# Performance work log

Measured on AMD Instinct MI355X. Metric: run time of the kernel, lower is better.

The kernel has to match this reference:

```python
import jax, jax.numpy as jnp
import numpy as np

MUL = 8              # multiplicity of 0e and 1o irreps (feature dim = MUL + 3*MUL = 32)
N_NODES = 25000
N_EDGES = 200000
EDGE_ATTR_DIM = 16
RADIAL_HIDDEN = 64
N_PATHS = 5          # CG paths: 0e*0e->0e, 0e*1o->1o, 1o*0e->1o, 1o*1o->0e, 1o*1o->1o


def _split(x):
    # x: [*, MUL + 3*MUL] -> scalars [*, MUL], vectors [*, MUL, 3]
    return x[:, :MUL], x[:, MUL:].reshape(x.shape[0], MUL, 3)


def _radial(edge_attr, W1, W2):
    # two-layer radial net (e3nn FullyConnectedNet style, silu, fan-in normalized)
    h = jax.nn.silu(edge_attr @ W1 / jnp.sqrt(float(EDGE_ATTR_DIM)))
    w = h @ W2 / jnp.sqrt(float(RADIAL_HIDDEN))
    return w.reshape(-1, N_PATHS, MUL, MUL)  # [E, 5, MUL, MUL]


def _edge_tp(xs, xv, s0, s1, w):
    # per-edge FullyConnectedTensorProduct(irreps_in, irreps_sh, irreps_out)
    # xs:[E,MUL] xv:[E,MUL,3] s0:[E] s1:[E,3] w:[E,5,MUL,MUL]
    dot = jnp.einsum('emc,ec->em', xv, s1) / jnp.sqrt(3.0)          # 1o x 1o -> 0e
    out_s = (jnp.einsum('emn,em->en', w[:, 0], xs) * s0[:, None]
             + jnp.einsum('emn,em->en', w[:, 3], dot)) / jnp.sqrt(2.0 * MUL)
    cross = jnp.cross(xv, s1[:, None, :]) / jnp.sqrt(2.0)            # 1o x 1o -> 1o
    out_v = (jnp.einsum('emn,em->en', w[:, 1], xs)[:, :, None] * s1[:, None, :]
             + jnp.einsum('emn,emc->enc', w[:, 2], xv) * s0[:, None, None]
             + jnp.einsum('emn,emc->enc', w[:, 4], cross)) / jnp.sqrt(3.0 * MUL)
    return out_s, out_v


def setup_inputs() -> dict:
    key = jax.random.key(0)
    ks = jax.random.split(key, 12)
    node_attr = jax.random.normal(ks[0], (N_NODES, 4 * MUL), jnp.float32)
    edge_index = jax.random.randint(ks[1], (2, N_EDGES), 0, N_NODES, dtype=jnp.int32)
    edge_attr = jax.random.normal(ks[2], (N_EDGES, EDGE_ATTR_DIM), jnp.float32)
    edge_sh = jax.random.normal(ks[3], (N_EDGES, 4), jnp.float32)
    WSZ = N_PATHS * MUL * MUL
    return {
        'node_attr': node_attr,
        'edge_index': edge_index,
        'edge_attr': edge_attr,
        'edge_sh': edge_sh,
        'Wq0': jax.random.normal(ks[4], (MUL, MUL), jnp.float32),
        'Wq1': jax.random.normal(ks[5], (MUL, MUL), jnp.float32),
        'kW1': jax.random.normal(ks[6], (EDGE_ATTR_DIM, RADIAL_HIDDEN), jnp.float32),
        'kW2': jax.random.normal(ks[7], (RADIAL_HIDDEN, WSZ), jnp.float32),
        'vW1': jax.random.normal(ks[8], (EDGE_ATTR_DIM, RADIAL_HIDDEN), jnp.float32),
        'vW2': jax.random.normal(ks[9], (RADIAL_HIDDEN, WSZ), jnp.float32),
        'Wd0': jax.random.normal(ks[10], (MUL, MUL), jnp.float32),
        'Wd1': jax.random.normal(ks[11], (MUL, MUL), jnp.float32),
    }


def reference(node_attr, edge_index, edge_attr, edge_sh,
              Wq0, Wq1, kW1, kW2, vW1, vW2, Wd0, Wd1):
    src, dst = edge_index[0], edge_index[1]
    inv_sqrt_mul = 1.0 / jnp.sqrt(float(MUL))

    # q = o3.Linear(irreps_in -> irreps_query): mixes multiplicities within each irrep
    ns, nv = _split(node_attr)
    qs = ns @ Wq0 * inv_sqrt_mul                                   # [N, MUL]
    qv = jnp.einsum('nmc,mk->nkc', nv, Wq1) * inv_sqrt_mul          # [N, MUL, 3]

    # per-edge keys/values: gather src features, tensor product with edge_sh
    xs, xv = ns[src], nv[src]
    s0, s1 = edge_sh[:, 0], edge_sh[:, 1:4]
    wk = _radial(edge_attr, kW1, kW2)
    wv = _radial(edge_attr, vW1, vW2)
    ks_, kv_ = _edge_tp(xs, xv, s0, s1, wk)
    vs_, vv_ = _edge_tp(xs, xv, s0, s1, wv)

    # dot = FullyConnectedTensorProduct(query, key, '0e') per edge
    logits = (jnp.einsum('mn,em,en->e', Wd0, qs[dst], ks_)
              + jnp.einsum('mn,emc,enc->e', Wd1, qv[dst], kv_) / jnp.sqrt(3.0)
              ) / jnp.sqrt(2.0 * MUL)
    exp = jnp.exp(logits)[:, None]                                 # [E, 1]

    # scatter-mean normalization
    z_sum = jax.ops.segment_sum(exp, dst, num_segments=N_NODES)
    cnt = jax.ops.segment_sum(jnp.ones_like(exp), dst, num_segments=N_NODES)
    z = z_sum / jnp.maximum(cnt, 1.0)
    alpha = exp / z[dst]
    attn = jnp.sqrt(jax.nn.relu(alpha))

    # weighted scatter-sum aggregation
    v_edge = jnp.concatenate([vs_, vv_.reshape(-1, 3 * MUL)], axis=1)  # [E, 32]
    out = jax.ops.segment_sum(attn * v_edge, dst, num_segments=N_NODES)
    return out
```

## Files before the change

### kernel.cpp

```cpp
#include <hip/hip_runtime.h>
#include <math.h>

#define NE 200000
#define NN 25000

static constexpr float INV_SQRT3  = 0.5773502691896258f;
static constexpr float INV_SQRT2  = 0.7071067811865476f;
static constexpr float INV_SQRT8  = 0.3535533905932738f;
static constexpr float INV_SQRT24 = 0.2041241452319315f;

typedef __attribute__((ext_vector_type(8))) short bf16x8;
typedef __attribute__((ext_vector_type(4))) float f32x4;

union U16x8 { uint4 u; bf16x8 v; };

__device__ __forceinline__ unsigned f2bf1(float f) {
  unsigned u = __float_as_uint(f);
  return (u + 0x7FFFu + ((u >> 16) & 1u)) >> 16;
}
__device__ __forceinline__ unsigned packbf(float a, float b) {
  return f2bf1(a) | (f2bf1(b) << 16);
}
__device__ __forceinline__ float bflo(unsigned u) { return __uint_as_float(u << 16); }
__device__ __forceinline__ float bfhi(unsigned u) { return __uint_as_float(u & 0xFFFF0000u); }

__global__ __launch_bounds__(256) void prep_kernel(
    const float* __restrict__ kW1, const float* __restrict__ kW2,
    const float* __restrict__ vW1, const float* __restrict__ vW2,
    const float* __restrict__ node_attr,
    const float* __restrict__ Wq0, const float* __restrict__ Wq1,
    const float* __restrict__ Wd0, const float* __restrict__ Wd1,
    const int*   __restrict__ edge_index,
    unsigned short* __restrict__ afrag,
    unsigned short* __restrict__ afrag1,
    float* __restrict__ qd, float* __restrict__ qvd,
    int* __restrict__ hist)
{
  int t = blockIdx.x * blockDim.x + threadIdx.x;
  if (t < 4096) {
    int j    = t & 7;
    int lane = (t >> 3) & 63;
    int rt   = (t >> 9) & 3;
    int b    = (t >> 11) & 1;
    int quad = lane >> 4;
    int k    = quad * 8 + j;
    int jeff = k & 15;
    int r    = rt * 16 + (lane & 15);
    const float* W = b ? vW1 : kW1;
    afrag1[t] = (unsigned short)f2bf1(W[jeff * 64 + r]);
  }
  if (t < 40960) {
    int j    = t & 7;
    int lane = (t >> 3) & 63;
    int kk   = (t >> 9) & 1;
    int ot   = (t >> 10) & 1;
    int ci   = t >> 11;
    int b    = ci / 10;
    int rem  = ci - b * 10;
    int p    = rem >> 1;
    int hf   = rem & 1;
    int r    = kk * 32 + ((lane >> 4) << 3) + j;
    int o    = p * 64 + hf * 32 + ot * 16 + (lane & 15);
    const float* W = b ? vW2 : kW2;
    afrag[t] = (unsigned short)f2bf1(W[r * 320 + o]);
  }
#pragma unroll
  for (int i = 0; i < 5; ++i) {
    int e = t * 5 + i;
    if (e < NE) atomicAdd(&hist[edge_index[NE + e]], 1);
  }
  if (t < NN) {
    int n = t;
    float ns[8], nv[24];
#pragma unroll
    for (int i = 0; i < 8; ++i)  ns[i] = node_attr[n * 32 + i];
#pragma unroll
    for (int i = 0; i < 24; ++i) nv[i] = node_attr[n * 32 + 8 + i];
    float qs[8];
#pragma unroll
    for (int m = 0; m < 8; ++m) {
      float a = 0.f;
#pragma unroll
      for (int i = 0; i < 8; ++i) a = fmaf(ns[i], Wq0[i * 8 + m], a);
      qs[m] = a * INV_SQRT8;
    }
#pragma unroll
    for (int k = 0; k < 8; ++k) {
      float a = 0.f;
#pragma unroll
      for (int m = 0; m < 8; ++m) a = fmaf(qs[m], Wd0[m * 8 + k], a);
      qd[n * 8 + k] = a;
    }
    float qv[24];
#pragma unroll
    for (int k = 0; k < 8; ++k) {
#pragma unroll
      for (int c = 0; c < 3; ++c) {
        float a = 0.f;
#pragma unroll
        for (int m = 0; m < 8; ++m) a = fmaf(nv[m * 3 + c], Wq1[m * 8 + k], a);
        qv[k * 3 + c] = a * INV_SQRT8;
      }
    }
#pragma unroll
    for (int k = 0; k < 8; ++k) {
#pragma unroll
      for (int c = 0; c < 3; ++c) {
        float a = 0.f;
#pragma unroll
        for (int m = 0; m < 8; ++m) a = fmaf(qv[m * 3 + c], Wd1[m * 8 + k], a);
        qvd[n * 24 + k * 3 + c] = a;
      }
    }
  }
}

__global__ __launch_bounds__(1024) void scan_kernel(
    const int* __restrict__ hist, int* __restrict__ off, int* __restrict__ cursor)
{
  __shared__ int wsum[16];
  const int tid  = threadIdx.x;
  const int lane = tid & 63;
  const int wv   = tid >> 6;
  const int base = tid * 25;
  int loc[25];
  int s = 0;
#pragma unroll
  for (int i = 0; i < 25; ++i) {
    int idx = base + i;
    int v = (idx < NN) ? hist[idx] : 0;
    loc[i] = s;
    s += v;
  }
  int incl = s;
#pragma unroll
  for (int d = 1; d < 64; d <<= 1) {
    int t = __shfl_up(incl, d, 64);
    if (lane >= d) incl += t;
  }
  int wexcl = incl - s;
  if (lane == 63) wsum[wv] = incl;
  __syncthreads();
  if (wv == 0 && lane < 16) {
    int v = wsum[lane];
    int inc2 = v;
#pragma unroll
    for (int d = 1; d < 16; d <<= 1) {
      int t = __shfl_up(inc2, d, 64);
      if (lane >= d) inc2 += t;
    }
    wsum[lane] = inc2 - v;
  }
  __syncthreads();
  int tbase = wsum[wv] + wexcl;
#pragma unroll
  for (int i = 0; i < 25; ++i) {
    int idx = base + i;
    if (idx < NN) { int e = tbase + loc[i]; off[idx] = e; cursor[idx] = e; }
  }
  if (tid == 1023) off[NN] = tbase + s;
}

__global__ __launch_bounds__(256) void edge_kernel(
    const float* __restrict__ node_attr,
    const int*   __restrict__ edge_index,
    const float* __restrict__ edge_attr,
    const float* __restrict__ edge_sh,
    const unsigned short* __restrict__ afrag1,
    const unsigned short* __restrict__ afrag,
    const float* __restrict__ qd,   const float* __restrict__ qvd,
    int* __restrict__ cursor,
    float* __restrict__ exo, float* __restrict__ wout)
{
  __shared__ unsigned char smem[36864];
  const int tid  = threadIdx.x;
  const int lane = tid & 63;
  const int wave = tid >> 6;
  const int l15  = lane & 15;
  const int quad = lane >> 4;
  unsigned char* reg9k = smem + wave * 9216;
  unsigned char* sea = reg9k;
  unsigned char* sh  = reg9k;
  unsigned char* swp = reg9k;

  const int e = blockIdx.x * 256 + tid;
  const bool valid = (e < NE);
  const int el  = valid ? e : (NE - 1);
  const int src = edge_index[el];
  const int dst = edge_index[NE + el];

  int pos = 0;
  if (valid) pos = atomicAdd(&cursor[dst], 1);

  const float s0  = edge_sh[el * 4 + 0];
  const float s1x = edge_sh[el * 4 + 1];
  const float s1y = edge_sh[el * 4 + 2];
  const float s1z = edge_sh[el * 4 + 3];

  {
    float ea[16];
    const float4* ea4 = (const float4*)(edge_attr + (size_t)el * 16);
#pragma unroll
    for (int i = 0; i < 4; ++i) {
      float4 v = ea4[i];
      ea[4*i+0] = v.x; ea[4*i+1] = v.y; ea[4*i+2] = v.z; ea[4*i+3] = v.w;
    }
    unsigned char* myrow = sea + lane * 80;
    unsigned hi[8];
    float lo[16];
#pragma unroll
    for (int i = 0; i < 8; ++i) {
      unsigned h0 = f2bf1(ea[2*i]);
      unsigned h1 = f2bf1(ea[2*i+1]);
      hi[i] = h0 | (h1 << 16);
      lo[2*i]   = ea[2*i]   - bflo(h0);
      lo[2*i+1] = ea[2*i+1] - bflo(h1);
    }
    uint4 w0 = {hi[0], hi[1], hi[2], hi[3]};
    uint4 w1 = {hi[4], hi[5], hi[6], hi[7]};
    *(uint4*)(myrow)      = w0;
    *(uint4*)(myrow + 16) = w1;
    uint4 w2, w3;
    w2.x = packbf(lo[0], lo[1]);   w2.y = packbf(lo[2], lo[3]);
    w2.z = packbf(lo[4], lo[5]);   w2.w = packbf(lo[6], lo[7]);
    w3.x = packbf(lo[8], lo[9]);   w3.y = packbf(lo[10], lo[11]);
    w3.z = packbf(lo[12], lo[13]); w3.w = packbf(lo[14], lo[15]);
    *(uint4*)(myrow + 32) = w2;
    *(uint4*)(myrow + 48) = w3;
  }

  U16x8 B1[4];
#pragma unroll
  for (int et = 0; et < 4; ++et)
    B1[et].u = *(const uint4*)(sea + (et*16 + l15) * 80 + quad * 16);

  float xs[8], xv[8][3];
  {
    const float4* na4 = (const float4*)(node_attr + (size_t)src * 32);
    float tmp[32];
#pragma unroll
    for (int i = 0; i < 8; ++i) {
      float4 v = na4[i];
      tmp[4*i+0] = v.x; tmp[4*i+1] = v.y; tmp[4*i+2] = v.z; tmp[4*i+3] = v.w;
    }
#pragma unroll
    for (int m = 0; m < 8; ++m) xs[m] = tmp[m];
#pragma unroll
    for (int m = 0; m < 8; ++m) {
      xv[m][0] = tmp[8 + 3*m + 0];
      xv[m][1] = tmp[8 + 3*m + 1];
      xv[m][2] = tmp[8 + 3*m + 2];
    }
  }

  const uint4* AF  = (const uint4*)afrag;
  const uint4* AF1 = (const uint4*)afrag1;
  float ex = 0.f;

#pragma unroll 1
  for (int b = 0; b < 2; ++b) {
#pragma unroll 1
    for (int rt = 0; rt < 4; ++rt) {
      U16x8 a1;
      a1.u = AF1[(b * 4 + rt) * 64 + lane];
#pragma unroll
      for (int et = 0; et < 4; ++et) {
        f32x4 c = {0.f, 0.f, 0.f, 0.f};
        c = __builtin_amdgcn_mfma_f32_16x16x32_bf16(a1.v, B1[et].v, c, 0, 0, 0);
        float hh[4];
#pragma unroll
        for (int i = 0; i < 4; ++i) {
          float x = c[i] * 0.25f;
          hh[i] = x / (1.f + __expf(-x));
        }
        uint2 pk;
        pk.x = packbf(hh[0], hh[1]);
        pk.y = packbf(hh[2], hh[3]);
        *(uint2*)(sh + (et*16 + l15) * 144 + (rt*16 + quad*4) * 2) = pk;
      }
    }

    bf16x8 B[4][2];
#pragma unroll
    for (int et = 0; et < 4; ++et) {
#pragma unroll
      for (int kk = 0; kk < 2; ++kk) {
        U16x8 cv;
        cv.u = *(const uint4*)(sh + (et*16 + l15) * 144 + kk * 64 + quad * 16);
        B[et][kk] = cv.v;
      }
    }

    float accs[8];
    float accv[8][3];
#pragma unroll
    for (int n = 0; n < 8; ++n) {
      accs[n] = 0.f;
      accv[n][0] = 0.f; accv[n][1] = 0.f; accv[n][2] = 0.f;
    }

#pragma unroll 1
    for (int cc = 0; cc < 10; ++cc) {
      const int p  = cc >> 1;
      const int hf = cc & 1;
      const int ci = b * 10 + cc;
      U16x8 a00, a01, a10, a11;
      a00.u = AF[(ci*4 + 0) * 64 + lane];
      a01.u = AF[(ci*4 + 1) * 64 + lane];
      a10.u = AF[(ci*4 + 2) * 64 + lane];
      a11.u = AF[(ci*4 + 3) * 64 + lane];

#pragma unroll
      for (int et = 0; et < 4; ++et) {
        f32x4 c0 = {0.f, 0.f, 0.f, 0.f};
        f32x4 c1 = {0.f, 0.f, 0.f, 0.f};
        c0 = __builtin_amdgcn_mfma_f32_16x16x32_bf16(a00.v, B[et][0], c0, 0, 0, 0);
        c0 = __builtin_amdgcn_mfma_f32_16x16x32_bf16(a01.v, B[et][1], c0, 0, 0, 0);
        c1 = __builtin_amdgcn_mfma_f32_16x16x32_bf16(a10.v, B[et][0], c1, 0, 0, 0);
        c1 = __builtin_amdgcn_mfma_f32_16x16x32_bf16(a11.v, B[et][1], c1, 0, 0, 0);
        unsigned char* wrow = swp + (et*16 + l15) * 80;
        uint2 p0; p0.x = packbf(c0.x, c0.y); p0.y = packbf(c0.z, c0.w);
        uint2 p1; p1.x = packbf(c1.x, c1.y); p1.y = packbf(c1.z, c1.w);
        *(uint2*)(wrow + quad * 8)      = p0;
        *(uint2*)(wrow + 32 + quad * 8) = p1;
      }

      const uint4* wr = (const uint4*)(swp + (size_t)lane * 80);
#pragma unroll
      for (int h2 = 0; h2 < 2; ++h2) {
        uint4 qa = wr[h2 * 2], qb = wr[h2 * 2 + 1];
        float wvv[16];
        {
          unsigned qs_[8] = {qa.x,qa.y,qa.z,qa.w, qb.x,qb.y,qb.z,qb.w};
#pragma unroll
          for (int i = 0; i < 8; ++i) {
            wvv[2*i]   = bflo(qs_[i]);
            wvv[2*i+1] = bfhi(qs_[i]);
          }
        }
#pragma unroll
        for (int mm = 0; mm < 2; ++mm) {
          const int m = hf * 4 + h2 * 2 + mm;
          const float* wm = &wvv[mm * 8];
          if (p == 0) {
            float g = xs[m] * s0;
#pragma unroll
            for (int n = 0; n < 8; ++n) accs[n] = fmaf(wm[n], g, accs[n]);
          } else if (p == 1) {
            float a = xs[m];
            float gx = a * s1x, gy = a * s1y, gz = a * s1z;
#pragma unroll
            for (int n = 0; n < 8; ++n) {
              accv[n][0] = fmaf(wm[n], gx, accv[n][0]);
              accv[n][1] = fmaf(wm[n], gy, accv[n][1]);
              accv[n][2] = fmaf(wm[n], gz, accv[n][2]);
            }
          } else if (p == 2) {
            float gx = xv[m][0] * s0, gy = xv[m][1] * s0, gz = xv[m][2] * s0;
#pragma unroll
            for (int n = 0; n < 8; ++n) {
              accv[n][0] = fmaf(wm[n], gx, accv[n][0]);
              accv[n][1] = fmaf(wm[n], gy, accv[n][1]);
              accv[n][2] = fmaf(wm[n], gz, accv[n][2]);
            }
          } else if (p == 3) {
            float dm = (xv[m][0]*s1x + xv[m][1]*s1y + xv[m][2]*s1z) * INV_SQRT3;
#pragma unroll
            for (int n = 0; n < 8; ++n) accs[n] = fmaf(wm[n], dm, accs[n]);
          } else {
            float crx = (xv[m][1]*s1z - xv[m][2]*s1y) * INV_SQRT2;
            float cry = (xv[m][2]*s1x - xv[m][0]*s1z) * INV_SQRT2;
            float crz = (xv[m][0]*s1y - xv[m][1]*s1x) * INV_SQRT2;
#pragma unroll
            for (int n = 0; n < 8; ++n) {
              accv[n][0] = fmaf(wm[n], crx, accv[n][0]);
              accv[n][1] = fmaf(wm[n], cry, accv[n][1]);
              accv[n][2] = fmaf(wm[n], crz, accv[n][2]);
            }
          }
        }
      }
    }

    if (b == 0) {
      float lg = 0.f, lv = 0.f;
#pragma unroll
      for (int n = 0; n < 8; ++n) lg = fmaf(accs[n], qd[dst * 8 + n], lg);
#pragma unroll
      for (int n = 0; n < 8; ++n) {
#pragma unroll
        for (int c = 0; c < 3; ++c)
          lv = fmaf(accv[n][c], qvd[dst * 24 + n * 3 + c], lv);
      }
      float logit = (lg * (1.f / 32.f) +
                     lv * (0.125f * INV_SQRT24) * INV_SQRT3) * 0.25f;
      ex = __expf(logit);
      if (valid) exo[pos] = ex;
    } else {
      if (valid) {
        float a = sqrtf(ex);
        const float ss = a * (1.f / 32.f);
        const float sv = a * (0.125f * INV_SQRT24);
        float4* v4 = (float4*)(wout + (size_t)pos * 32);
        float4 o;
        o.x = accs[0] * ss; o.y = accs[1] * ss;
        o.z = accs[2] * ss; o.w = accs[3] * ss;
        v4[0] = o;
        o.x = accs[4] * ss; o.y = accs[5] * ss;
        o.z = accs[6] * ss; o.w = accs[7] * ss;
        v4[1] = o;
        o.x = accv[0][0] * sv; o.y = accv[0][1] * sv;
        o.z = accv[0][2] * sv; o.w = accv[1][0] * sv;
        v4[2] = o;
        o.x = accv[1][1] * sv; o.y = accv[1][2] * sv;
        o.z = accv[2][0] * sv; o.w = accv[2][1] * sv;
        v4[3] = o;
        o.x = accv[2][2] * sv; o.y = accv[3][0] * sv;
        o.z = accv[3][1] * sv; o.w = accv[3][2] * sv;
        v4[4] = o;
        o.x = accv[4][0] * sv; o.y = accv[4][1] * sv;
        o.z = accv[4][2] * sv; o.w = accv[5][0] * sv;
        v4[5] = o;
        o.x = accv[5][1] * sv; o.y = accv[5][2] * sv;
        o.z = accv[6][0] * sv; o.w = accv[6][1] * sv;
        v4[6] = o;
        o.x = accv[6][2] * sv; o.y = accv[7][0] * sv;
        o.z = accv[7][1] * sv; o.w = accv[7][2] * sv;
        v4[7] = o;
      }
    }
  }
}

__global__ __launch_bounds__(256) void gather_kernel(
    const int* __restrict__ off,
    const float* __restrict__ exo,
    const float* __restrict__ wout,
    float* __restrict__ out)
{
  const int tid  = threadIdx.x;
  const int wave = tid >> 6;
  const int lane = tid & 63;
  const int n = blockIdx.x * 4 + wave;
  if (n >= NN) return;
  const int start = off[n];
  const int end   = off[n + 1];
  const int cnt   = end - start;

  float zp = 0.f;
  for (int j = start + lane; j < end; j += 64) zp += exo[j];
#pragma unroll
  for (int s = 32; s >= 1; s >>= 1) zp += __shfl_xor(zp, s, 64);

  const int l  = lane & 31;
  const int hh = lane >> 5;
  float acc = 0.f;
  for (int j = start + hh; j < end; j += 2)
    acc += wout[(size_t)j * 32 + l];
  acc += __shfl_xor(acc, 32, 64);

  if (lane < 32) {
    float s = (cnt > 0 && zp > 0.f) ? sqrtf((float)cnt / zp) : 0.f;
    out[(size_t)n * 32 + l] = acc * s;
  }
}

extern "C" void kernel_launch(void* const* d_in, const int* in_sizes, int n_in,
                              void* d_out, int out_size, void* d_ws, size_t ws_size,
                              hipStream_t stream)
{
  const float* node_attr  = (const float*)d_in[0];
  const int*   edge_index = (const int*)  d_in[1];
  const float* edge_attr  = (const float*)d_in[2];
  const float* edge_sh    = (const float*)d_in[3];
  const float* Wq0 = (const float*)d_in[4];
  const float* Wq1 = (const float*)d_in[5];
  const float* kW1 = (const float*)d_in[6];
  const float* kW2 = (const float*)d_in[7];
  const float* vW1 = (const float*)d_in[8];
  const float* vW2 = (const float*)d_in[9];
  const float* Wd0 = (const float*)d_in[10];
  const float* Wd1 = (const float*)d_in[11];
  float* out = (float*)d_out;

  float* ws = (float*)d_ws;
  float* qd     = ws;
  float* qvd    = qd   + 200000;
  unsigned short* afrag  = (unsigned short*)(qvd + 600000);
  unsigned short* afrag1 = afrag + 40960;
  int* hist   = (int*)(afrag1 + 4096);
  int* off    = hist + 25024;
  int* cursor = off  + 25056;
  float* exo  = (float*)(cursor + 25024);
  float* wout = exo + 200000;

  hipMemsetAsync(hist, 0, 25024 * sizeof(int), stream);

  prep_kernel<<<160, 256, 0, stream>>>(
      kW1, kW2, vW1, vW2, node_attr, Wq0, Wq1, Wd0, Wd1, edge_index,
      afrag, afrag1, qd, qvd, hist);
  scan_kernel<<<1, 1024, 0, stream>>>(hist, off, cursor);
  edge_kernel<<<(NE + 255) / 256, 256, 0, stream>>>(
      node_attr, edge_index, edge_attr, edge_sh,
      afrag1, afrag, qd, qvd, cursor, exo, wout);
  gather_kernel<<<(NN + 3) / 4, 256, 0, stream>>>(off, exo, wout, out);
}
```

Baseline: 247.7 us.

## Factor edge-sh out of TP accumulation, prefetch MFMA fragments, vectorize gather

```diff
diff --git a/kernel.cpp b/kernel.cpp
--- a/kernel.cpp
+++ b/kernel.cpp
@@ -1,4 +1,5 @@
 #include <hip/hip_runtime.h>
+#include <hip/hip_bf16.h>
 #include <math.h>
 
 #define NE 200000
@@ -19,7 +20,9 @@
   return (u + 0x7FFFu + ((u >> 16) & 1u)) >> 16;
 }
 __device__ __forceinline__ unsigned packbf(float a, float b) {
-  return f2bf1(a) | (f2bf1(b) << 16);
+  union { __hip_bfloat162 h; unsigned u; } c;
+  c.h = __float22bfloat162_rn(make_float2(a, b));
+  return c.u;
 }
 __device__ __forceinline__ float bflo(unsigned u) { return __uint_as_float(u << 16); }
 __device__ __forceinline__ float bfhi(unsigned u) { return __uint_as_float(u & 0xFFFF0000u); }
@@ -210,11 +213,10 @@
     float lo[16];
 #pragma unroll
     for (int i = 0; i < 8; ++i) {
-      unsigned h0 = f2bf1(ea[2*i]);
-      unsigned h1 = f2bf1(ea[2*i+1]);
-      hi[i] = h0 | (h1 << 16);
-      lo[2*i]   = ea[2*i]   - bflo(h0);
-      lo[2*i+1] = ea[2*i+1] - bflo(h1);
+      unsigned pk = packbf(ea[2*i], ea[2*i+1]);
+      hi[i] = pk;
+      lo[2*i]   = ea[2*i]   - bflo(pk);
+      lo[2*i+1] = ea[2*i+1] - bfhi(pk);
     }
     uint4 w0 = {hi[0], hi[1], hi[2], hi[3]};
     uint4 w1 = {hi[4], hi[5], hi[6], hi[7]};
@@ -291,33 +293,44 @@
       }
     }
 
-    float accs[8];
-    float accv[8][3];
+    float T0[8], T1[8], T3[8];
+    float U2[8][3], U4[8][3];
 #pragma unroll
     for (int n = 0; n < 8; ++n) {
-      accs[n] = 0.f;
-      accv[n][0] = 0.f; accv[n][1] = 0.f; accv[n][2] = 0.f;
-    }
-
+      T0[n] = 0.f; T1[n] = 0.f; T3[n] = 0.f;
+      U2[n][0] = 0.f; U2[n][1] = 0.f; U2[n][2] = 0.f;
+      U4[n][0] = 0.f; U4[n][1] = 0.f; U4[n][2] = 0.f;
+    }
+
+    U16x8 a0, a1_, a2, a3;
+    {
+      const int ci = b * 10;
+      a0.u  = AF[(ci*4 + 0) * 64 + lane];
+      a1_.u = AF[(ci*4 + 1) * 64 + lane];
+      a2.u  = AF[(ci*4 + 2) * 64 + lane];
+      a3.u  = AF[(ci*4 + 3) * 64 + lane];
+    }
 #pragma unroll 1
     for (int cc = 0; cc < 10; ++cc) {
       const int p  = cc >> 1;
       const int hf = cc & 1;
-      const int ci = b * 10 + cc;
-      U16x8 a00, a01, a10, a11;
-      a00.u = AF[(ci*4 + 0) * 64 + lane];
-      a01.u = AF[(ci*4 + 1) * 64 + lane];
-      a10.u = AF[(ci*4 + 2) * 64 + lane];
-      a11.u = AF[(ci*4 + 3) * 64 + lane];
+      U16x8 n0, n1, n2, n3;
+      {
+        const int cn = b * 10 + (cc < 9 ? cc + 1 : 9);
+        n0.u = AF[(cn*4 + 0) * 64 + lane];
+        n1.u = AF[(cn*4 + 1) * 64 + lane];
+        n2.u = AF[(cn*4 + 2) * 64 + lane];
+        n3.u = AF[(cn*4 + 3) * 64 + lane];
+      }
 
 #pragma unroll
       for (int et = 0; et < 4; ++et) {
         f32x4 c0 = {0.f, 0.f, 0.f, 0.f};
         f32x4 c1 = {0.f, 0.f, 0.f, 0.f};
-        c0 = __builtin_amdgcn_mfma_f32_16x16x32_bf16(a00.v, B[et][0], c0, 0, 0, 0);
-        c0 = __builtin_amdgcn_mfma_f32_16x16x32_bf16(a01.v, B[et][1], c0, 0, 0, 0);
-        c1 = __builtin_amdgcn_mfma_f32_16x16x32_bf16(a10.v, B[et][0], c1, 0, 0, 0);
-        c1 = __builtin_amdgcn_mfma_f32_16x16x32_bf16(a11.v, B[et][1], c1, 0, 0, 0);
+        c0 = __builtin_amdgcn_mfma_f32_16x16x32_bf16(a0.v,  B[et][0], c0, 0, 0, 0);
+        c0 = __builtin_amdgcn_mfma_f32_16x16x32_bf16(a1_.v, B[et][1], c0, 0, 0, 0);
+        c1 = __builtin_amdgcn_mfma_f32_16x16x32_bf16(a2.v,  B[et][0], c1, 0, 0, 0);
+        c1 = __builtin_amdgcn_mfma_f32_16x16x32_bf16(a3.v,  B[et][1], c1, 0, 0, 0);
         unsigned char* wrow = swp + (et*16 + l15) * 80;
         uint2 p0; p0.x = packbf(c0.x, c0.y); p0.y = packbf(c0.z, c0.w);
         uint2 p1; p1.x = packbf(c1.x, c1.y); p1.y = packbf(c1.z, c1.w);
@@ -343,54 +356,57 @@
           const int m = hf * 4 + h2 * 2 + mm;
           const float* wm = &wvv[mm * 8];
           if (p == 0) {
-            float g = xs[m] * s0;
-#pragma unroll
-            for (int n = 0; n < 8; ++n) accs[n] = fmaf(wm[n], g, accs[n]);
+            const float g = xs[m];
+#pragma unroll
+            for (int n = 0; n < 8; ++n) T0[n] = fmaf(wm[n], g, T0[n]);
           } else if (p == 1) {
-            float a = xs[m];
-            float gx = a * s1x, gy = a * s1y, gz = a * s1z;
+            const float g = xs[m];
+#pragma unroll
+            for (int n = 0; n < 8; ++n) T1[n] = fmaf(wm[n], g, T1[n]);
+          } else if (p == 2) {
+            const float g0 = xv[m][0], g1 = xv[m][1], g2 = xv[m][2];
 #pragma unroll
             for (int n = 0; n < 8; ++n) {
-              accv[n][0] = fmaf(wm[n], gx, accv[n][0]);
-              accv[n][1] = fmaf(wm[n], gy, accv[n][1]);
-              accv[n][2] = fmaf(wm[n], gz, accv[n][2]);
-            }
-          } else if (p == 2) {
-            float gx = xv[m][0] * s0, gy = xv[m][1] * s0, gz = xv[m][2] * s0;
-#pragma unroll
-            for (int n = 0; n < 8; ++n) {
-              accv[n][0] = fmaf(wm[n], gx, accv[n][0]);
-              accv[n][1] = fmaf(wm[n], gy, accv[n][1]);
-              accv[n][2] = fmaf(wm[n], gz, accv[n][2]);
+              U2[n][0] = fmaf(wm[n], g0, U2[n][0]);
+              U2[n][1] = fmaf(wm[n], g1, U2[n][1]);
+              U2[n][2] = fmaf(wm[n], g2, U2[n][2]);
             }
           } else if (p == 3) {
             float dm = (xv[m][0]*s1x + xv[m][1]*s1y + xv[m][2]*s1z) * INV_SQRT3;
 #pragma unroll
-            for (int n = 0; n < 8; ++n) accs[n] = fmaf(wm[n], dm, accs[n]);
+            for (int n = 0; n < 8; ++n) T3[n] = fmaf(wm[n], dm, T3[n]);
           } else {
-            float crx = (xv[m][1]*s1z - xv[m][2]*s1y) * INV_SQRT2;
-            float cry = (xv[m][2]*s1x - xv[m][0]*s1z) * INV_SQRT2;
-            float crz = (xv[m][0]*s1y - xv[m][1]*s1x) * INV_SQRT2;
+            const float g0 = xv[m][0], g1 = xv[m][1], g2 = xv[m][2];
 #pragma unroll
             for (int n = 0; n < 8; ++n) {
-              accv[n][0] = fmaf(wm[n], crx, accv[n][0]);
-              accv[n][1] = fmaf(wm[n], cry, accv[n][1]);
-              accv[n][2] = fmaf(wm[n], crz, accv[n][2]);
+              U4[n][0] = fmaf(wm[n], g0, U4[n][0]);
+              U4[n][1] = fmaf(wm[n], g1, U4[n][1]);
+              U4[n][2] = fmaf(wm[n], g2, U4[n][2]);
             }
           }
         }
       }
+      a0 = n0; a1_ = n1; a2 = n2; a3 = n3;
     }
 
     if (b == 0) {
       float lg = 0.f, lv = 0.f;
 #pragma unroll
-      for (int n = 0; n < 8; ++n) lg = fmaf(accs[n], qd[dst * 8 + n], lg);
-#pragma unroll
       for (int n = 0; n < 8; ++n) {
-#pragma unroll
-        for (int c = 0; c < 3; ++c)
-          lv = fmaf(accv[n][c], qvd[dst * 24 + n * 3 + c], lv);
+        float as = fmaf(T0[n], s0, T3[n]);
+        lg = fmaf(as, qd[dst * 8 + n], lg);
+      }
+#pragma unroll
+      for (int n = 0; n < 8; ++n) {
+        float cx = (U4[n][1]*s1z - U4[n][2]*s1y) * INV_SQRT2;
+        float cy = (U4[n][2]*s1x - U4[n][0]*s1z) * INV_SQRT2;
+        float cz = (U4[n][0]*s1y - U4[n][1]*s1x) * INV_SQRT2;
+        float a0v = T1[n]*s1x + U2[n][0]*s0 + cx;
+        float a1v = T1[n]*s1y + U2[n][1]*s0 + cy;
+        float a2v = T1[n]*s1z + U2[n][2]*s0 + cz;
+        lv = fmaf(a0v, qvd[dst*24 + n*3 + 0], lv);
+        lv = fmaf(a1v, qvd[dst*24 + n*3 + 1], lv);
+        lv = fmaf(a2v, qvd[dst*24 + n*3 + 2], lv);
       }
       float logit = (lg * (1.f / 32.f) +
                      lv * (0.125f * INV_SQRT24) * INV_SQRT3) * 0.25f;
@@ -401,31 +417,34 @@
         float a = sqrtf(ex);
         const float ss = a * (1.f / 32.f);
         const float sv = a * (0.125f * INV_SQRT24);
+        float accs[8], accv[8][3];
+#pragma unroll
+        for (int n = 0; n < 8; ++n) {
+          accs[n] = fmaf(T0[n], s0, T3[n]) * ss;
+          float cx = (U4[n][1]*s1z - U4[n][2]*s1y) * INV_SQRT2;
+          float cy = (U4[n][2]*s1x - U4[n][0]*s1z) * INV_SQRT2;
+          float cz = (U4[n][0]*s1y - U4[n][1]*s1x) * INV_SQRT2;
+          accv[n][0] = (T1[n]*s1x + U2[n][0]*s0 + cx) * sv;
+          accv[n][1] = (T1[n]*s1y + U2[n][1]*s0 + cy) * sv;
+          accv[n][2] = (T1[n]*s1z + U2[n][2]*s0 + cz) * sv;
+        }
         float4* v4 = (float4*)(wout + (size_t)pos * 32);
         float4 o;
-        o.x = accs[0] * ss; o.y = accs[1] * ss;
-        o.z = accs[2] * ss; o.w = accs[3] * ss;
+        o.x = accs[0]; o.y = accs[1]; o.z = accs[2]; o.w = accs[3];
         v4[0] = o;
-        o.x = accs[4] * ss; o.y = accs[5] * ss;
-        o.z = accs[6] * ss; o.w = accs[7] * ss;
+        o.x = accs[4]; o.y = accs[5]; o.z = accs[6]; o.w = accs[7];
         v4[1] = o;
-        o.x = accv[0][0] * sv; o.y = accv[0][1] * sv;
-        o.z = accv[0][2] * sv; o.w = accv[1][0] * sv;
+        o.x = accv[0][0]; o.y = accv[0][1]; o.z = accv[0][2]; o.w = accv[1][0];
         v4[2] = o;
-        o.x = accv[1][1] * sv; o.y = accv[1][2] * sv;
-        o.z = accv[2][0] * sv; o.w = accv[2][1] * sv;
+        o.x = accv[1][1]; o.y = accv[1][2]; o.z = accv[2][0]; o.w = accv[2][1];
         v4[3] = o;
-        o.x = accv[2][2] * sv; o.y = accv[3][0] * sv;
-        o.z = accv[3][1] * sv; o.w = accv[3][2] * sv;
+        o.x = accv[2][2]; o.y = accv[3][0]; o.z = accv[3][1]; o.w = accv[3][2];
         v4[4] = o;
-        o.x = accv[4][0] * sv; o.y = accv[4][1] * sv;
-        o.z = accv[4][2] * sv; o.w = accv[5][0] * sv;
+        o.x = accv[4][0]; o.y = accv[4][1]; o.z = accv[4][2]; o.w = accv[5][0];
         v4[5] = o;
-        o.x = accv[5][1] * sv; o.y = accv[5][2] * sv;
-        o.z = accv[6][0] * sv; o.w = accv[6][1] * sv;
+        o.x = accv[5][1]; o.y = accv[5][2]; o.z = accv[6][0]; o.w = accv[6][1];
         v4[6] = o;
-        o.x = accv[6][2] * sv; o.y = accv[7][0] * sv;
-        o.z = accv[7][1] * sv; o.w = accv[7][2] * sv;
+        o.x = accv[6][2]; o.y = accv[7][0]; o.z = accv[7][1]; o.w = accv[7][2];
         v4[7] = o;
       }
     }
@@ -452,16 +471,25 @@
 #pragma unroll
   for (int s = 32; s >= 1; s >>= 1) zp += __shfl_xor(zp, s, 64);
 
-  const int l  = lane & 31;
-  const int hh = lane >> 5;
-  float acc = 0.f;
-  for (int j = start + hh; j < end; j += 2)
-    acc += wout[(size_t)j * 32 + l];
-  acc += __shfl_xor(acc, 32, 64);
-
-  if (lane < 32) {
+  const int q  = lane & 7;
+  const int rr = lane >> 3;
+  float4 acc = {0.f, 0.f, 0.f, 0.f};
+  const float4* w4 = (const float4*)wout;
+  for (int j = start + rr; j < end; j += 8) {
+    float4 v = w4[(size_t)j * 8 + q];
+    acc.x += v.x; acc.y += v.y; acc.z += v.z; acc.w += v.w;
+  }
+#pragma unroll
+  for (int s = 8; s < 64; s <<= 1) {
+    acc.x += __shfl_xor(acc.x, s, 64);
+    acc.y += __shfl_xor(acc.y, s, 64);
+    acc.z += __shfl_xor(acc.z, s, 64);
+    acc.w += __shfl_xor(acc.w, s, 64);
+  }
+  if (rr == 0) {
     float s = (cnt > 0 && zp > 0.f) ? sqrtf((float)cnt / zp) : 0.f;
-    out[(size_t)n * 32 + l] = acc * s;
+    float4 o = {acc.x * s, acc.y * s, acc.z * s, acc.w * s};
+    ((float4*)out)[(size_t)n * 8 + q] = o;
   }
 }
 
```

Result: slower. 408.3 us (+64.8%).
